# Kernel tuning notes

Measured on AMD Instinct MI355X. Metric: run time of the kernel, lower is better.

## Reference

```python
import jax, jax.numpy as jnp
import numpy as np

D_MODEL = 1024
N_HEADS = 16
MAX_LEN = 2048
B, T = 2, 2048


def _rope_tables(seq_len, d_model):
    # NOTE: inv_freq spans full d_model (not d_head), matching the source module,
    # since RoPE is applied to q/k of shape (B, T, D) before the head split.
    inv_freq = 1.0 / 10000 ** (jnp.arange(0, d_model, 2, dtype=jnp.float32) / d_model)
    pos = jnp.arange(seq_len, dtype=jnp.float32)
    freqs = jnp.outer(pos, inv_freq)            # (T, D/2)
    return jnp.cos(freqs), jnp.sin(freqs)


def _apply_rope(x, cos, sin):
    # x: (B, T, D); cos/sin: (T, D/2)
    c = jnp.repeat(cos, 2, axis=-1)[None]       # (1, T, D)
    s = jnp.repeat(sin, 2, axis=-1)[None]
    xr = x.reshape(x.shape[0], x.shape[1], -1, 2)
    x_rot = jnp.stack([-xr[..., 1], xr[..., 0]], axis=-1).reshape(x.shape)
    return x * c + x_rot * s


def setup_inputs() -> dict:
    key = jax.random.key(0)
    ks = jax.random.split(key, 5)
    scale = 1.0 / np.sqrt(D_MODEL)
    x = jax.random.normal(ks[0], (B, T, D_MODEL), dtype=jnp.float32)
    wq = jax.random.normal(ks[1], (D_MODEL, D_MODEL), dtype=jnp.float32) * scale
    wk = jax.random.normal(ks[2], (D_MODEL, D_MODEL), dtype=jnp.float32) * scale
    wv = jax.random.normal(ks[3], (D_MODEL, D_MODEL), dtype=jnp.float32) * scale
    wo = jax.random.normal(ks[4], (D_MODEL, D_MODEL), dtype=jnp.float32) * scale
    mask = jnp.tril(jnp.ones((T, T), dtype=bool))[None, None]  # (1,1,T,T) causal
    return {"x": x, "mask": mask, "wq": wq, "wk": wk, "wv": wv, "wo": wo}


def reference(x, mask, wq, wk, wv, wo):
    Bn, Tn, Dn = x.shape
    d_head = Dn // N_HEADS
    cos, sin = _rope_tables(Tn, Dn)
    q = _apply_rope(x @ wq, cos, sin)
    k = _apply_rope(x @ wk, cos, sin)
    v = x @ wv
    q = q.reshape(Bn, Tn, N_HEADS, d_head).transpose(0, 2, 1, 3)  # (B,H,T,dh)
    k = k.reshape(Bn, Tn, N_HEADS, d_head).transpose(0, 2, 1, 3)
    v = v.reshape(Bn, Tn, N_HEADS, d_head).transpose(0, 2, 1, 3)
    scores = jnp.einsum('bhqd,bhkd->bhqk', q, k) / jnp.sqrt(jnp.float32(d_head))
    scores = jnp.where(mask, scores, jnp.float32(-1e10))
    attn = jax.nn.softmax(scores, axis=-1)
    out = jnp.einsum('bhqk,bhkd->bhqd', attn, v)
    out = out.transpose(0, 2, 1, 3).reshape(Bn, Tn, Dn)
    return out @ wo
```

## Files before the change

kernel.cpp:

```cpp
#include <hip/hip_runtime.h>
#include <hip/hip_bf16.h>

#define D_MODEL 1024
#define N_HEADS 16
#define DH      64
#define BATCH   2
#define SEQ     2048
#define M_ROWS  (BATCH*SEQ)

using f32x4  = __attribute__((ext_vector_type(4)))  float;
using f32x16 = __attribute__((ext_vector_type(16))) float;
using bfx8   = __attribute__((ext_vector_type(8)))  short;

__device__ __forceinline__ float bf2f(unsigned short u){
    unsigned int v = ((unsigned int)u) << 16;
    float f; __builtin_memcpy(&f, &v, 4); return f;
}
__device__ __forceinline__ unsigned short f2bf(float f){
    unsigned int u; __builtin_memcpy(&u, &f, 4);
    u = (u + 0x7FFFu + ((u >> 16) & 1u)) >> 16;
    return (unsigned short)u;
}
__device__ __forceinline__ unsigned int cvtpk_bf16(float lo, float hi){
    unsigned int r;
    asm("v_cvt_pk_bf16_f32 %0, %1, %2" : "=v"(r) : "v"(lo), "v"(hi));
    return r;
}

typedef __attribute__((address_space(3))) void as3_void;
typedef __attribute__((address_space(1))) const void as1_cvoid;
__device__ __forceinline__ void gload16(const void* g, void* l){
    __builtin_amdgcn_global_load_lds((as1_cvoid*)g, (as3_void*)l, 16, 0, 0);
}

__global__ void cast_x_kernel(const float* __restrict__ x, unsigned short* __restrict__ xb){
    int i = blockIdx.x*blockDim.x + threadIdx.x;
    float4 v = reinterpret_cast<const float4*>(x)[i];
    ushort4 o; o.x=f2bf(v.x); o.y=f2bf(v.y); o.z=f2bf(v.z); o.w=f2bf(v.w);
    reinterpret_cast<ushort4*>(xb)[i] = o;
}

__global__ void transpose_cast_w(const float* __restrict__ w0, const float* __restrict__ w1,
                                 const float* __restrict__ w2, const float* __restrict__ w3,
                                 unsigned short* __restrict__ o0, unsigned short* __restrict__ o1,
                                 unsigned short* __restrict__ o2, unsigned short* __restrict__ o3){
    __shared__ float tile[32][33];
    const float* w; unsigned short* o;
    switch (blockIdx.z){
        case 0:  w=w0; o=o0; break;
        case 1:  w=w1; o=o1; break;
        case 2:  w=w2; o=o2; break;
        default: w=w3; o=o3; break;
    }
    const int tx = threadIdx.x, ty = threadIdx.y;
    const int x0 = blockIdx.x*32, y0 = blockIdx.y*32;
    #pragma unroll
    for (int j=0;j<32;j+=8) tile[ty+j][tx] = w[(size_t)(y0+ty+j)*D_MODEL + x0 + tx];
    __syncthreads();
    #pragma unroll
    for (int j=0;j<32;j+=8) o[(size_t)(x0+ty+j)*D_MODEL + y0 + tx] = f2bf(tile[tx][ty+j]);
}

__global__ __launch_bounds__(256) void gemm_qkv(const unsigned short* __restrict__ A,
                                                const unsigned short* __restrict__ Bq,
                                                const unsigned short* __restrict__ Bk,
                                                const unsigned short* __restrict__ Bv,
                                                unsigned short* __restrict__ Qo,
                                                unsigned short* __restrict__ Ko,
                                                unsigned short* __restrict__ Vto){
    __shared__ unsigned short As[64*64];
    __shared__ unsigned short Bs[128*64];
    const int sel = blockIdx.x >> 3;
    const int n0  = (blockIdx.x & 7) * 128;
    const unsigned short* Bt = (sel==0) ? Bq : ((sel==1) ? Bk : Bv);
    const int tid = threadIdx.x;
    const int lane = tid & 63, wid = tid >> 6;
    const int l15 = lane & 15, hi = lane >> 4;
    const int wr = wid >> 1, wc = wid & 1;
    const int m0 = blockIdx.y * 64;

    f32x4 acc[2][4] = {};

    for (int kt = 0; kt < D_MODEL; kt += 64){
        __syncthreads();
        #pragma unroll
        for (int i = 0; i < 2; ++i){
            int c = tid + 256*i;
            int row = c >> 3, ch = c & 7;
            int sc = ch ^ (row & 7);
            gload16(A + (size_t)(m0 + row)*D_MODEL + kt + sc*8, As + c*8);
        }
        #pragma unroll
        for (int i = 0; i < 4; ++i){
            int c = tid + 256*i;
            int row = c >> 3, ch = c & 7;
            int sc = ch ^ (row & 7);
            gload16(Bt + (size_t)(n0 + row)*D_MODEL + kt + sc*8, Bs + c*8);
        }
        asm volatile("s_waitcnt vmcnt(0)" ::: "memory");
        __syncthreads();
        #pragma unroll
        for (int ks = 0; ks < 2; ++ks){
            bfx8 a[2], b[4];
            #pragma unroll
            for (int t = 0; t < 2; ++t){
                const int ra = 32*wr + 16*t + l15;
                a[t] = *reinterpret_cast<const bfx8*>(As + ra*64 + (((ks*4 + hi) ^ (ra & 7))*8));
            }
            #pragma unroll
            for (int t = 0; t < 4; ++t){
                const int rb = 64*wc + 16*t + l15;
                b[t] = *reinterpret_cast<const bfx8*>(Bs + rb*64 + (((ks*4 + hi) ^ (rb & 7))*8));
            }
            #pragma unroll
            for (int rt = 0; rt < 2; ++rt)
                #pragma unroll
                for (int ct = 0; ct < 4; ++ct)
                    acc[rt][ct] = __builtin_amdgcn_mfma_f32_16x16x32_bf16(a[rt], b[ct], acc[rt][ct], 0, 0, 0);
        }
    }

    if (sel < 2){
        unsigned short* o = sel ? Ko : Qo;
        const float cfac = -0.02595256269f;
        float invf[4];
        #pragma unroll
        for (int ct = 0; ct < 4; ++ct){
            const int n = n0 + 64*wc + 16*ct + l15;
            invf[ct] = exp2f(cfac * (float)(n >> 1));
        }
        #pragma unroll
        for (int rt = 0; rt < 2; ++rt)
            #pragma unroll
            for (int ct = 0; ct < 4; ++ct){
                const int m = m0 + 32*wr + 16*rt + 4*hi;
                const int n = n0 + 64*wc + 16*ct + l15;
                #pragma unroll
                for (int r=0;r<4;++r){
                    float v = acc[rt][ct][r];
                    float prt = __shfl_xor(v, 1);
                    int tpos = (m + r) & (SEQ-1);
                    float ang = (float)tpos * invf[ct];
                    float sv = __sinf(ang), cv = __cosf(ang);
                    float rot = (n & 1) ? __builtin_fmaf(v, cv,  prt*sv)
                                        : __builtin_fmaf(v, cv, -(prt*sv));
                    o[(size_t)(m+r)*D_MODEL + n] = f2bf(rot);
                }
            }
    } else {
        #pragma unroll
        for (int rt = 0; rt < 2; ++rt)
            #pragma unroll
            for (int ct = 0; ct < 4; ++ct){
                const int m = m0 + 32*wr + 16*rt + 4*hi;
                const int n = n0 + 64*wc + 16*ct + l15;
                const int b  = m >> 11, t = m & (SEQ-1);
                const int h  = n >> 6,  d = n & 63;
                ushort4 pk;
                pk.x = f2bf(acc[rt][ct][0]); pk.y = f2bf(acc[rt][ct][1]);
                pk.z = f2bf(acc[rt][ct][2]); pk.w = f2bf(acc[rt][ct][3]);
                *reinterpret_cast<ushort4*>(Vto + ((size_t)((b*N_HEADS + h)*DH + d))*SEQ + t) = pk;
            }
    }
}

__global__ __launch_bounds__(256) void gemm_out(const unsigned short* __restrict__ A,
                                                const unsigned short* __restrict__ Bt,
                                                float* __restrict__ dst){
    __shared__ unsigned short As[64*64];
    __shared__ unsigned short Bs[128*64];
    const int tid = threadIdx.x;
    const int lane = tid & 63, wid = tid >> 6;
    const int l15 = lane & 15, hi = lane >> 4;
    const int wr = wid >> 1, wc = wid & 1;
    const int m0 = blockIdx.y * 64, n0 = blockIdx.x * 128;

    f32x4 acc[2][4] = {};

    for (int kt = 0; kt < D_MODEL; kt += 64){
        __syncthreads();
        #pragma unroll
        for (int i = 0; i < 2; ++i){
            int c = tid + 256*i;
            int row = c >> 3, ch = c & 7;
            int sc = ch ^ (row & 7);
            gload16(A + (size_t)(m0 + row)*D_MODEL + kt + sc*8, As + c*8);
        }
        #pragma unroll
        for (int i = 0; i < 4; ++i){
            int c = tid + 256*i;
            int row = c >> 3, ch = c & 7;
            int sc = ch ^ (row & 7);
            gload16(Bt + (size_t)(n0 + row)*D_MODEL + kt + sc*8, Bs + c*8);
        }
        asm volatile("s_waitcnt vmcnt(0)" ::: "memory");
        __syncthreads();
        #pragma unroll
        for (int ks = 0; ks < 2; ++ks){
            bfx8 a[2], b[4];
            #pragma unroll
            for (int t = 0; t < 2; ++t){
                const int ra = 32*wr + 16*t + l15;
                a[t] = *reinterpret_cast<const bfx8*>(As + ra*64 + (((ks*4 + hi) ^ (ra & 7))*8));
            }
            #pragma unroll
            for (int t = 0; t < 4; ++t){
                const int rb = 64*wc + 16*t + l15;
                b[t] = *reinterpret_cast<const bfx8*>(Bs + rb*64 + (((ks*4 + hi) ^ (rb & 7))*8));
            }
            #pragma unroll
            for (int rt = 0; rt < 2; ++rt)
                #pragma unroll
                for (int ct = 0; ct < 4; ++ct)
                    acc[rt][ct] = __builtin_amdgcn_mfma_f32_16x16x32_bf16(a[rt], b[ct], acc[rt][ct], 0, 0, 0);
        }
    }

    #pragma unroll
    for (int rt = 0; rt < 2; ++rt)
        #pragma unroll
        for (int ct = 0; ct < 4; ++ct){
            const int m = m0 + 32*wr + 16*rt + 4*hi;
            const int n = n0 + 64*wc + 16*ct + l15;
            #pragma unroll
            for (int r=0;r<4;++r) dst[(size_t)(m+r)*D_MODEL + n] = acc[rt][ct][r];
        }
}

__global__ __launch_bounds__(256, 2) void attn_kernel(const unsigned short* __restrict__ Q,
                                                      const unsigned short* __restrict__ K,
                                                      const unsigned short* __restrict__ Vt,
                                                      unsigned short* __restrict__ O){
    __shared__ float Olds[3][64][64];
    __shared__ float Llds[3][64];

    const int tid = threadIdx.x;
    const int lane = tid & 63, wid = tid >> 6;
    const int l31 = lane & 31, hi2 = (lane >> 5) & 1;
    const int bid = blockIdx.x;
    const int xcd = bid & 7, j = bid >> 3;
    const int hp  = xcd*4 + (j & 3);
    const int b = hp >> 4, h = hp & 15;
    const int qt2 = 31 - (j >> 2);
    const int skmax = 2*qt2 + 1;
    const int qrowA = qt2*64 + l31;
    const int qrowB = qrowA + 32;

    const unsigned short* Kbase = K  + (size_t)(b*SEQ)*D_MODEL + h*DH + 8*hi2;
    const unsigned short* Vbase = Vt + ((size_t)((b*N_HEADS + h)*DH))*SEQ + 8*hi2;
    const float k2 = 0.18033688011f;

    bfx8 qfA[4], qfB[4];
    {
        const unsigned short* qa = Q + ((size_t)(b*SEQ) + qrowA)*D_MODEL + h*DH + 8*hi2;
        const unsigned short* qb = Q + ((size_t)(b*SEQ) + qrowB)*D_MODEL + h*DH + 8*hi2;
        #pragma unroll
        for (int m=0;m<4;++m){
            qfA[m] = *reinterpret_cast<const bfx8*>(qa + 16*m);
            qfB[m] = *reinterpret_cast<const bfx8*>(qb + 16*m);
        }
    }

    f32x16 oaccA[2] = {}, oaccB[2] = {};
    float lA = 0.f, lB = 0.f;

    bfx8 kf[4];
    if (wid <= skmax){
        const unsigned short* kp = Kbase + (size_t)(wid*32 + l31)*D_MODEL;
        #pragma unroll
        for (int m=0;m<4;++m) kf[m] = *reinterpret_cast<const bfx8*>(kp + 16*m);
    }

    for (int sk = wid; sk <= skmax; sk += 4){
        bfx8 vf[2][2];
        #pragma unroll
        for (int dt=0; dt<2; ++dt)
            #pragma unroll
            for (int ks=0; ks<2; ++ks)
                vf[dt][ks] = *reinterpret_cast<const bfx8*>(Vbase + (size_t)(32*dt + l31)*SEQ + sk*32 + 16*ks);

        const bool doA = (sk < skmax);

        f32x16 stA = {}, stB = {};
        __builtin_amdgcn_s_setprio(1);
        #pragma unroll
        for (int m=0; m<4; ++m){
            if (doA) stA = __builtin_amdgcn_mfma_f32_32x32x16_bf16(kf[m], qfA[m], stA, 0,0,0);
            stB = __builtin_amdgcn_mfma_f32_32x32x16_bf16(kf[m], qfB[m], stB, 0,0,0);
        }
        __builtin_amdgcn_s_setprio(0);

        bfx8 kn[4];
        if (sk + 4 <= skmax){
            const unsigned short* kp = Kbase + (size_t)((sk+4)*32 + l31)*D_MODEL;
            #pragma unroll
            for (int m=0;m<4;++m) kn[m] = *reinterpret_cast<const bfx8*>(kp + 16*m);
        }

        float pA[16], pB[16];
        float rsA = 0.f, rsB = 0.f;
        const bool maskA = (sk == 2*qt2);
        const bool maskB = (sk == skmax);
        #pragma unroll
        for (int r=0;r<16;++r){
            int kg = sk*32 + (r&3) + 8*(r>>2) + 4*hi2;
            if (doA){
                float eA = (maskA && kg > qrowA) ? 0.f : exp2f(stA[r]*k2);
                pA[r] = eA; rsA += eA;
            }
            float eB = (maskB && kg > qrowB) ? 0.f : exp2f(stB[r]*k2);
            pB[r] = eB; rsB += eB;
        }
        if (doA){ rsA += __shfl_xor(rsA, 32); lA += rsA; }
        rsB += __shfl_xor(rsB, 32); lB += rsB;

        bfx8 paA0, paA1, paB0, paB1;
        if (doA){
            unsigned int c[8], x[8];
            #pragma unroll
            for (int q=0;q<8;++q) c[q] = cvtpk_bf16(pA[2*q], pA[2*q+1]);
            #pragma unroll
            for (int q=0;q<8;++q) x[q] = __shfl_xor(c[q], 32);
            uint4 w0 = (hi2==0) ? make_uint4(c[0],c[1],x[0],x[1]) : make_uint4(x[2],x[3],c[2],c[3]);
            uint4 w1 = (hi2==0) ? make_uint4(c[4],c[5],x[4],x[5]) : make_uint4(x[6],x[7],c[6],c[7]);
            paA0 = *reinterpret_cast<bfx8*>(&w0);
            paA1 = *reinterpret_cast<bfx8*>(&w1);
        }
        {
            unsigned int c[8], x[8];
            #pragma unroll
            for (int q=0;q<8;++q) c[q] = cvtpk_bf16(pB[2*q], pB[2*q+1]);
            #pragma unroll
            for (int q=0;q<8;++q) x[q] = __shfl_xor(c[q], 32);
            uint4 w0 = (hi2==0) ? make_uint4(c[0],c[1],x[0],x[1]) : make_uint4(x[2],x[3],c[2],c[3]);
            uint4 w1 = (hi2==0) ? make_uint4(c[4],c[5],x[4],x[5]) : make_uint4(x[6],x[7],c[6],c[7]);
            paB0 = *reinterpret_cast<bfx8*>(&w0);
            paB1 = *reinterpret_cast<bfx8*>(&w1);
        }

        __builtin_amdgcn_s_setprio(1);
        #pragma unroll
        for (int dt=0; dt<2; ++dt){
            if (doA){
                f32x16 o = oaccA[dt];
                o = __builtin_amdgcn_mfma_f32_32x32x16_bf16(paA0, vf[dt][0], o, 0,0,0);
                o = __builtin_amdgcn_mfma_f32_32x32x16_bf16(paA1, vf[dt][1], o, 0,0,0);
                oaccA[dt] = o;
            }
            f32x16 o = oaccB[dt];
            o = __builtin_amdgcn_mfma_f32_32x32x16_bf16(paB0, vf[dt][0], o, 0,0,0);
            o = __builtin_amdgcn_mfma_f32_32x32x16_bf16(paB1, vf[dt][1], o, 0,0,0);
            oaccB[dt] = o;
        }
        __builtin_amdgcn_s_setprio(0);

        #pragma unroll
        for (int m=0;m<4;++m) kf[m] = kn[m];
    }

    if (wid != 0){
        #pragma unroll
        for (int r=0; r<16; ++r){
            const int crow = (r&3) + 8*(r>>2) + 4*hi2;
            #pragma unroll
            for (int dt=0; dt<2; ++dt){
                Olds[wid-1][crow     ][32*dt + l31] = oaccA[dt][r];
                Olds[wid-1][crow + 32][32*dt + l31] = oaccB[dt][r];
            }
        }
        if (hi2 == 0){ Llds[wid-1][l31] = lA; Llds[wid-1][l31 + 32] = lB; }
    }
    __syncthreads();
    if (wid == 0){
        float la = lA, lb = lB;
        #pragma unroll
        for (int jj=0;jj<3;++jj){ la += Llds[jj][l31]; lb += Llds[jj][l31 + 32]; }
        float invA = 1.0f / la, invB = 1.0f / lb;
        #pragma unroll
        for (int r=0; r<16; ++r){
            const int crow = (r&3) + 8*(r>>2) + 4*hi2;
            float icA = __shfl(invA, crow);
            float icB = __shfl(invB, crow);
            #pragma unroll
            for (int dt=0; dt<2; ++dt){
                float va = oaccA[dt][r], vb = oaccB[dt][r];
                #pragma unroll
                for (int jj=0;jj<3;++jj){
                    va += Olds[jj][crow     ][32*dt + l31];
                    vb += Olds[jj][crow + 32][32*dt + l31];
                }
                const int rowA = qt2*64 + crow;
                O[((size_t)(b*SEQ) + rowA     )*D_MODEL + h*DH + 32*dt + l31] = f2bf(va * icA);
                O[((size_t)(b*SEQ) + rowA + 32)*D_MODEL + h*DH + 32*dt + l31] = f2bf(vb * icB);
            }
        }
    }
}

extern "C" void kernel_launch(void* const* d_in, const int* in_sizes, int n_in,
                              void* d_out, int out_size, void* d_ws, size_t ws_size,
                              hipStream_t stream) {
    const float* x  = (const float*)d_in[0];
    const float* wq = (const float*)d_in[2];
    const float* wk = (const float*)d_in[3];
    const float* wv = (const float*)d_in[4];
    const float* wo = (const float*)d_in[5];

    char* ws = (char*)d_ws;
    unsigned short* xb  = (unsigned short*)(ws);
    unsigned short* wqt = (unsigned short*)(ws + (8u  << 20));
    unsigned short* wkt = (unsigned short*)(ws + (10u << 20));
    unsigned short* wvt = (unsigned short*)(ws + (12u << 20));
    unsigned short* wot = (unsigned short*)(ws + (14u << 20));
    unsigned short* Qb  = (unsigned short*)(ws + (16u << 20));
    unsigned short* Kb  = (unsigned short*)(ws + (24u << 20));
    unsigned short* Vt  = (unsigned short*)(ws + (32u << 20));
    unsigned short* Ob  = (unsigned short*)(ws + (40u << 20));

    cast_x_kernel<<<M_ROWS*D_MODEL/4/256, 256, 0, stream>>>(x, xb);
    transpose_cast_w<<<dim3(32,32,4), dim3(32,8), 0, stream>>>(wq,wk,wv,wo, wqt,wkt,wvt,wot);

    gemm_qkv<<<dim3(24,64), 256, 0, stream>>>(xb, wqt, wkt, wvt, Qb, Kb, Vt);

    attn_kernel<<<1024, 256, 0, stream>>>(Qb, Kb, Vt, Ob);

    gemm_out<<<dim3(8,64), 256, 0, stream>>>(Ob, wot, (float*)d_out);
}
```

Baseline: 117.9 us.

## Raise attention occupancy via serialized LDS reduction and balanced tile ordering

The attention kernel's launch bounds go from 2 to 4 blocks per CU. Shared memory shrinks from three per-wave output buffers to one, and waves 1-3 now add their partial O and l values into it one after another, separated by barriers. Block-to-query-tile mapping is reordered in quarters so heavy and light causal tiles are interleaved across the launch, for better load balance. The tighter register budget could force spills of the large MFMA accumulators, and the serialized reduction adds extra barriers.

```diff
diff --git a/kernel.cpp b/kernel.cpp
--- a/kernel.cpp
+++ b/kernel.cpp
@@ -227,21 +227,30 @@
         }
 }
 
-__global__ __launch_bounds__(256, 2) void attn_kernel(const unsigned short* __restrict__ Q,
+__global__ __launch_bounds__(256, 4) void attn_kernel(const unsigned short* __restrict__ Q,
                                                       const unsigned short* __restrict__ K,
                                                       const unsigned short* __restrict__ Vt,
                                                       unsigned short* __restrict__ O){
-    __shared__ float Olds[3][64][64];
-    __shared__ float Llds[3][64];
+    __shared__ float Olds[64][64];
+    __shared__ float Llds[64];
 
     const int tid = threadIdx.x;
     const int lane = tid & 63, wid = tid >> 6;
     const int l31 = lane & 31, hi2 = (lane >> 5) & 1;
     const int bid = blockIdx.x;
-    const int xcd = bid & 7, j = bid >> 3;
+    const int quarter = bid >> 8;
+    const int r8  = bid & 255;
+    const int xcd = r8 & 7, j = r8 >> 3;
     const int hp  = xcd*4 + (j & 3);
     const int b = hp >> 4, h = hp & 15;
-    const int qt2 = 31 - (j >> 2);
+    const int idx = j >> 2;
+    int qt2;
+    switch (quarter){
+        case 0:  qt2 = 31 - idx; break;
+        case 1:  qt2 = idx;      break;
+        case 2:  qt2 = 23 - idx; break;
+        default: qt2 = 8 + idx;  break;
+    }
     const int skmax = 2*qt2 + 1;
     const int qrowA = qt2*64 + l31;
     const int qrowB = qrowA + 32;
@@ -358,23 +367,48 @@
         for (int m=0;m<4;++m) kf[m] = kn[m];
     }
 
-    if (wid != 0){
+    if (wid == 1){
         #pragma unroll
         for (int r=0; r<16; ++r){
             const int crow = (r&3) + 8*(r>>2) + 4*hi2;
             #pragma unroll
             for (int dt=0; dt<2; ++dt){
-                Olds[wid-1][crow     ][32*dt + l31] = oaccA[dt][r];
-                Olds[wid-1][crow + 32][32*dt + l31] = oaccB[dt][r];
-            }
-        }
-        if (hi2 == 0){ Llds[wid-1][l31] = lA; Llds[wid-1][l31 + 32] = lB; }
+                Olds[crow     ][32*dt + l31] = oaccA[dt][r];
+                Olds[crow + 32][32*dt + l31] = oaccB[dt][r];
+            }
+        }
+        if (hi2 == 0){ Llds[l31] = lA; Llds[l31 + 32] = lB; }
+    }
+    __syncthreads();
+    if (wid == 2){
+        #pragma unroll
+        for (int r=0; r<16; ++r){
+            const int crow = (r&3) + 8*(r>>2) + 4*hi2;
+            #pragma unroll
+            for (int dt=0; dt<2; ++dt){
+                Olds[crow     ][32*dt + l31] += oaccA[dt][r];
+                Olds[crow + 32][32*dt + l31] += oaccB[dt][r];
+            }
+        }
+        if (hi2 == 0){ Llds[l31] += lA; Llds[l31 + 32] += lB; }
+    }
+    __syncthreads();
+    if (wid == 3){
+        #pragma unroll
+        for (int r=0; r<16; ++r){
+            const int crow = (r&3) + 8*(r>>2) + 4*hi2;
+            #pragma unroll
+            for (int dt=0; dt<2; ++dt){
+                Olds[crow     ][32*dt + l31] += oaccA[dt][r];
+                Olds[crow + 32][32*dt + l31] += oaccB[dt][r];
+            }
+        }
+        if (hi2 == 0){ Llds[l31] += lA; Llds[l31 + 32] += lB; }
     }
     __syncthreads();
     if (wid == 0){
-        float la = lA, lb = lB;
-        #pragma unroll
-        for (int jj=0;jj<3;++jj){ la += Llds[jj][l31]; lb += Llds[jj][l31 + 32]; }
+        float la = lA + Llds[l31];
+        float lb = lB + Llds[l31 + 32];
         float invA = 1.0f / la, invB = 1.0f / lb;
         #pragma unroll
         for (int r=0; r<16; ++r){
@@ -383,12 +417,8 @@
             float icB = __shfl(invB, crow);
             #pragma unroll
             for (int dt=0; dt<2; ++dt){
-                float va = oaccA[dt][r], vb = oaccB[dt][r];
-                #pragma unroll
-                for (int jj=0;jj<3;++jj){
-                    va += Olds[jj][crow     ][32*dt + l31];
-                    vb += Olds[jj][crow + 32][32*dt + l31];
-                }
+                float va = oaccA[dt][r] + Olds[crow     ][32*dt + l31];
+                float vb = oaccB[dt][r] + Olds[crow + 32][32*dt + l31];
                 const int rowA = qt2*64 + crow;
                 O[((size_t)(b*SEQ) + rowA     )*D_MODEL + h*DH + 32*dt + l31] = f2bf(va * icA);
                 O[((size_t)(b*SEQ) + rowA + 32)*D_MODEL + h*DH + 32*dt + l31] = f2bf(vb * icB);
```

After: 281.6 us. 139% more time.
